# Performance work log

Measured on AMD Instinct MI355X. Metric: run time of the kernel, lower is better.

Reference implementation:

```python
import jax, jax.numpy as jnp
import numpy as np

G, VPG, CPG, LPC = 32, 512, 1024, 3
N_VARS, N_CLAUSES = G * VPG, G * CPG
N_LITS = N_CLAUSES * LPC
FM, QM, ROUNDS = 128, 32, 4
EPS_NORM, EPS_LOG, EPS_SQRT = 1e-6, 1e-8, 1e-6


def _dense_init(key, fin, fout):
    w = jax.random.normal(key, (fin, fout), jnp.float32) * np.float32(np.sqrt(2.0 / (fin + fout)))
    return w, jnp.zeros((fout,), jnp.float32)


def setup_inputs():
    rng = np.random.default_rng(0)
    g_of_clause = np.repeat(np.arange(G), CPG)
    lit_clause = np.repeat(np.arange(N_CLAUSES), LPC).astype(np.int32)
    # each clause picks LPC variables from its own graph's variable block
    lit_var = (np.repeat(g_of_clause * VPG, LPC) + rng.integers(0, VPG, N_LITS)).astype(np.int32)
    lit_sign = (rng.integers(0, 2, N_LITS) * 2 - 1).astype(np.int32)  # +/-1 literal polarity
    variables_mask = np.repeat(np.arange(G), VPG).astype(np.int32)
    clauses_mask = g_of_clause.astype(np.int32)
    keys = jax.random.split(jax.random.key(0), 13)
    inp = dict(
        lit_var=jnp.asarray(lit_var), lit_sign=jnp.asarray(lit_sign), lit_clause=jnp.asarray(lit_clause),
        variables_mask=jnp.asarray(variables_mask), clauses_mask=jnp.asarray(clauses_mask),
        noise=jax.random.normal(keys[12], (ROUNDS, N_VARS, 4), jnp.float32),
    )
    dims = dict(vq=(FM + 4, 2 * QM, QM), cm=(FM + QM, 3 * FM, FM + QM), ug=(FM + 3 * QM, 2 * FM, FM), vo=(FM, FM, 1))
    ki = 0
    for name, (fin, hid, fout) in dims.items():
        for i, (a, b) in enumerate([(fin, hid), (hid, hid), (hid, fout)]):
            w, bb = _dense_init(keys[ki], a, b); ki += 1
            inp[f'{name}_w{i}'] = w
            inp[f'{name}_b{i}'] = bb
    return inp


def _mlp(x, ps):
    # repo MLP: (layer_count-1) hidden Dense with leaky_relu(0.2), linear output, no layer norm
    for w, b in ps[:-1]:
        x = jax.nn.leaky_relu(x @ w + b, negative_slope=0.2)
    w, b = ps[-1]
    return x @ w + b


def _zero_state(n, f):
    # one_hot(0) - 1/f, scaled by sqrt(f)*0.25
    oh = jnp.zeros((n, f), jnp.float32).at[:, 0].set(1.0)
    return (oh - 1.0 / f) * np.float32(np.sqrt(f) * 0.25)


def _forward(lit_var, lit_sign, lit_clause, variables_mask, clauses_mask, noise, params, checkpoint=False):
    p = list(params)
    vq = [(p[0], p[1]), (p[2], p[3]), (p[4], p[5])]
    cm = [(p[6], p[7]), (p[8], p[9]), (p[10], p[11])]
    ug = [(p[12], p[13]), (p[14], p[15]), (p[16], p[17])]
    vo = [(p[18], p[19]), (p[20], p[21]), (p[22], p[23])]
    seg_sum = jax.ops.segment_sum
    sgn = lit_sign.astype(jnp.float32)[:, None]          # [L,1] +/-1
    pos = (sgn > 0).astype(jnp.float32)
    neg = 1.0 - pos
    var_cnt = seg_sum(jnp.ones((N_VARS,), jnp.float32), variables_mask, G)
    cls_cnt = seg_sum(jnp.ones((N_CLAUSES,), jnp.float32), clauses_mask, G)

    def pair_norm(x, seg, cnt):
        mean = seg_sum(x, seg, G) / cnt[:, None]
        x = x - mean[seg]
        return x * jax.lax.rsqrt(jnp.mean(jnp.square(x), axis=-1, keepdims=True) + EPS_NORM)

    def clause_val(q):
        # softplus_loss: V_c = exp(-sum_{lit in c} softplus(sign * q[var]))  -> [N_CLAUSES, d]
        lit = jax.nn.softplus(q[lit_var] * sgn)
        return jnp.exp(-seg_sum(lit, lit_clause, N_CLAUSES))

    def body(carry, noise_t):
        variables, clause_state = carry
        v1 = jnp.concatenate([variables, noise_t], axis=-1)          # [V, FM+4]
        query = _mlp(v1, vq)                                          # [V, QM]

        def q_loss(q):
            cl = clause_val(q)
            return jnp.sum(cl), cl
        variables_grad, clauses_loss = jax.grad(q_loss, has_aux=True)(query)

        clause_data = _mlp(jnp.concatenate([clause_state, clauses_loss], axis=-1), cm)  # [C, FM+QM]
        vloss = clause_data[:, :QM]
        new_cv = pair_norm(clause_data[:, QM:], clauses_mask, cls_cnt) * 0.25
        clause_state = new_cv + 0.1 * clause_state

        contrib = vloss[lit_clause]                                   # [L, QM]
        loss_pos = seg_sum(contrib * pos, lit_var, N_VARS)            # A_pos @ vloss
        loss_neg = seg_sum(contrib * neg, lit_var, N_VARS)            # A_neg @ vloss

        unit = jnp.concatenate([variables, variables_grad, loss_pos, loss_neg], axis=-1)
        new_vars = pair_norm(_mlp(unit, ug), variables_mask, var_cnt) * 0.25
        variables = new_vars + 0.1 * variables

        logits = _mlp(variables, vo)                                  # [V, 1]
        v = clause_val(logits)
        per_clause = v * (-jnp.log(1.0 - v + EPS_LOG))                # softplus_mixed_loss
        per_graph = seg_sum(per_clause, clauses_mask, G)              # [G, 1]
        logit_loss = jnp.sum(jnp.sqrt(per_graph + EPS_SQRT))

        variables = jax.lax.stop_gradient(variables) * 0.2 + variables * 0.8
        clause_state = jax.lax.stop_gradient(clause_state) * 0.2 + clause_state * 0.8
        return (variables, clause_state), (logit_loss, logits)

    if checkpoint:
        body = jax.checkpoint(body)
    init = (_zero_state(N_VARS, FM), _zero_state(N_CLAUSES, FM))
    _, (step_losses, logits_seq) = jax.lax.scan(body, init, noise)
    return logits_seq[-1], jnp.sum(step_losses) / np.float32(ROUNDS)


def reference(lit_var, lit_sign, lit_clause, variables_mask, clauses_mask, noise,
              vq_w0, vq_b0, vq_w1, vq_b1, vq_w2, vq_b2,
              cm_w0, cm_b0, cm_w1, cm_b1, cm_w2, cm_b2,
              ug_w0, ug_b0, ug_w1, ug_b1, ug_w2, ug_b2,
              vo_w0, vo_b0, vo_w1, vo_b1, vo_w2, vo_b2):
    params = (vq_w0, vq_b0, vq_w1, vq_b1, vq_w2, vq_b2,
              cm_w0, cm_b0, cm_w1, cm_b1, cm_w2, cm_b2,
              ug_w0, ug_b0, ug_w1, ug_b1, ug_w2, ug_b2,
              vo_w0, vo_b0, vo_w1, vo_b1, vo_w2, vo_b2)
    return _forward(lit_var, lit_sign, lit_clause, variables_mask, clauses_mask, noise, params)
```

## Files before the change

kernel.cpp:

```cpp
#include <hip/hip_runtime.h>
#include <hip/hip_bf16.h>
#include <math.h>

#define NG     32
#define NVARS  16384
#define NCLS   32768
#define NLITS  98304
#define NROUNDS 4

typedef __attribute__((ext_vector_type(8))) short bf16x8;
typedef __attribute__((ext_vector_type(4))) float f32x4;

#define OFF_VAR    ((size_t)0)
#define OFF_CST    ((size_t)2097152)
#define OFF_XCMB   ((size_t)6291456)
#define OFF_XUGB   ((size_t)9437184)
#define OFF_ABUF   ((size_t)11534336)
#define OFF_BBUF   ((size_t)17825792)
#define OFF_CD     ((size_t)24117248)
#define OFF_Q      ((size_t)30408704)
#define OFF_VG     ((size_t)30932992)
#define OFF_LP     ((size_t)31457280)
#define OFF_LN     ((size_t)31981568)
#define OFF_CMEAN  ((size_t)32505856)
#define OFF_VMEAN  ((size_t)32509952)
#define ZERO_FLOATS ((size_t)1581056)
#define OFF_LOSS   ((size_t)32514048)
#define OFF_WT     ((size_t)32514052)

#define WT_CM0  ((size_t)0)
#define WT_CM1  ((size_t)73728)
#define WT_CM2  ((size_t)221184)
#define WT_UG0  ((size_t)294912)
#define WT_UG1  ((size_t)360448)
#define WT_UG2  ((size_t)425984)
#define WT_VO0  ((size_t)458752)
#define WT_VO1  ((size_t)475136)
#define WT_VQ0  ((size_t)491520)
#define WT_VQ1  ((size_t)501760)
#define WT_VQ2  ((size_t)505856)

__device__ __forceinline__ float softplus_f(float x) {
  return fmaxf(x, 0.f) + log1pf(expf(-fabsf(x)));
}
__device__ __forceinline__ short f2bf(float x) {
  __hip_bfloat16 h = __float2bfloat16(x);
  return *reinterpret_cast<short*>(&h);
}
__device__ __forceinline__ float bf2f(short s) {
  __hip_bfloat16 h = *reinterpret_cast<__hip_bfloat16*>(&s);
  return __bfloat162float(h);
}

__global__ void init_state_kernel(float* __restrict__ var, float* __restrict__ cst,
                                  short* __restrict__ xugb, short* __restrict__ xcmb,
                                  float* __restrict__ loss) {
  int t = blockIdx.x * blockDim.x + threadIdx.x;
  if (t == 0) *loss = 0.f;
  const int main_total = (NVARS + NCLS) * 128;
  if (t < main_total) {
    int row = t >> 7, m = t & 127;
    const float base = 2.82842712474619f;
    float val = ((m == 0) ? (1.f - 1.f / 128.f) : (-1.f / 128.f)) * base;
    if (row < NVARS) {
      var[(size_t)row * 128 + m] = val;
      xugb[(size_t)row * 256 + m] = f2bf(val);
    } else {
      int c = row - NVARS;
      cst[(size_t)c * 128 + m] = val;
      xcmb[(size_t)c * 192 + m] = f2bf(val);
    }
    return;
  }
  int t2 = t - main_total;
  if (t2 < NVARS * 32) {
    int row = t2 >> 5, j = t2 & 31;
    xugb[(size_t)row * 256 + 224 + j] = 0;
    return;
  }
  int t3 = t2 - NVARS * 32;
  if (t3 < NCLS * 32) {
    int row = t3 >> 5, j = t3 & 31;
    xcmb[(size_t)row * 192 + 160 + j] = 0;
  }
}

__global__ void convert_all_kernel(
    const float* __restrict__ cm_w0, const float* __restrict__ cm_w1, const float* __restrict__ cm_w2,
    const float* __restrict__ ug_w0, const float* __restrict__ ug_w1, const float* __restrict__ ug_w2,
    const float* __restrict__ vo_w0, const float* __restrict__ vo_w1,
    const float* __restrict__ vq_w0, const float* __restrict__ vq_w1, const float* __restrict__ vq_w2,
    short* __restrict__ wt) {
  int t = blockIdx.x * blockDim.x + threadIdx.x;
  const float* W; int K, N, Kp; size_t base; int idx;
  if      (t < 73728)  { W = cm_w0; K = 160; N = 384; Kp = 192; base = WT_CM0; idx = t; }
  else if (t < 221184) { W = cm_w1; K = 384; N = 384; Kp = 384; base = WT_CM1; idx = t - 73728; }
  else if (t < 294912) { W = cm_w2; K = 384; N = 160; Kp = 384; base = WT_CM2; idx = t - 221184; }
  else if (t < 360448) { W = ug_w0; K = 224; N = 256; Kp = 256; base = WT_UG0; idx = t - 294912; }
  else if (t < 425984) { W = ug_w1; K = 256; N = 256; Kp = 256; base = WT_UG1; idx = t - 360448; }
  else if (t < 458752) { W = ug_w2; K = 256; N = 128; Kp = 256; base = WT_UG2; idx = t - 425984; }
  else if (t < 475136) { W = vo_w0; K = 128; N = 128; Kp = 128; base = WT_VO0; idx = t - 458752; }
  else if (t < 491520) { W = vo_w1; K = 128; N = 128; Kp = 128; base = WT_VO1; idx = t - 475136; }
  else if (t < 501760) { W = vq_w0; K = 132; N = 64;  Kp = 160; base = WT_VQ0; idx = t - 491520; }
  else if (t < 505856) { W = vq_w1; K = 64;  N = 64;  Kp = 64;  base = WT_VQ1; idx = t - 501760; }
  else if (t < 507904) { W = vq_w2; K = 64;  N = 32;  Kp = 64;  base = WT_VQ2; idx = t - 505856; }
  else return;
  int n = idx / Kp, k = idx - n * Kp;
  float v = (k < K && n < N) ? W[(size_t)k * N + n] : 0.f;
  wt[base + idx] = f2bf(v);
}

__global__ __launch_bounds__(256) void fused_vq_kernel(
    const short* __restrict__ xugb, const float* __restrict__ noise,
    const short* __restrict__ w0, const short* __restrict__ w1, const short* __restrict__ w2,
    const float* __restrict__ b0, const float* __restrict__ b1, const float* __restrict__ b2,
    float* __restrict__ Q, float* __restrict__ zerobase) {
  {
    unsigned gid = blockIdx.x * 256 + threadIdx.x;
    float4 z4 = make_float4(0.f, 0.f, 0.f, 0.f);
    for (size_t i = gid; i < ZERO_FLOATS / 4; i += (size_t)(NVARS / 64) * 256)
      ((float4*)zerobase)[i] = z4;
  }
  __shared__ short A[64 * 160];
  __shared__ short H1[4][16 * 64];
  __shared__ short H2[4][16 * 64];
  const int wid = threadIdx.x >> 6, lane = threadIdx.x & 63;
  const int rbase = blockIdx.x * 64 + wid * 16;
  #pragma unroll
  for (int i = 0; i < 4; ++i) {
    int s = i * 64 + lane;
    int row = s >> 4, c8 = s & 15;
    *(bf16x8*)&A[(wid * 16 + row) * 160 + c8 * 8] =
        *(const bf16x8*)&xugb[(size_t)(rbase + row) * 256 + c8 * 8];
  }
  {
    int row = lane >> 2, seg = lane & 3;
    bf16x8 z = {0, 0, 0, 0, 0, 0, 0, 0};
    if (seg == 0) {
      float4 nz = *(const float4*)&noise[(size_t)(rbase + row) * 4];
      z[0] = f2bf(nz.x); z[1] = f2bf(nz.y); z[2] = f2bf(nz.z); z[3] = f2bf(nz.w);
    }
    *(bf16x8*)&A[(wid * 16 + row) * 160 + 128 + seg * 8] = z;
  }
  const int kof = (lane >> 4) * 8;
  const int l15 = lane & 15;
  f32x4 acc[4] = {};
  #pragma unroll
  for (int ks = 0; ks < 5; ++ks) {
    bf16x8 a = *(const bf16x8*)&A[(wid * 16 + l15) * 160 + ks * 32 + kof];
    #pragma unroll
    for (int ni = 0; ni < 4; ++ni) {
      bf16x8 b = *(const bf16x8*)&w0[(ni * 16 + l15) * 160 + ks * 32 + kof];
      acc[ni] = __builtin_amdgcn_mfma_f32_16x16x32_bf16(a, b, acc[ni], 0, 0, 0);
    }
  }
  #pragma unroll
  for (int ni = 0; ni < 4; ++ni) {
    int col = ni * 16 + l15;
    float bb = b0[col];
    #pragma unroll
    for (int j = 0; j < 4; ++j) {
      float v = acc[ni][j] + bb; v = v > 0.f ? v : 0.2f * v;
      H1[wid][((lane >> 4) * 4 + j) * 64 + col] = f2bf(v);
    }
  }
  f32x4 acc2[4] = {};
  #pragma unroll
  for (int ks = 0; ks < 2; ++ks) {
    bf16x8 a = *(const bf16x8*)&H1[wid][l15 * 64 + ks * 32 + kof];
    #pragma unroll
    for (int ni = 0; ni < 4; ++ni) {
      bf16x8 b = *(const bf16x8*)&w1[(ni * 16 + l15) * 64 + ks * 32 + kof];
      acc2[ni] = __builtin_amdgcn_mfma_f32_16x16x32_bf16(a, b, acc2[ni], 0, 0, 0);
    }
  }
  #pragma unroll
  for (int ni = 0; ni < 4; ++ni) {
    int col = ni * 16 + l15;
    float bb = b1[col];
    #pragma unroll
    for (int j = 0; j < 4; ++j) {
      float v = acc2[ni][j] + bb; v = v > 0.f ? v : 0.2f * v;
      H2[wid][((lane >> 4) * 4 + j) * 64 + col] = f2bf(v);
    }
  }
  f32x4 acc3[2] = {};
  #pragma unroll
  for (int ks = 0; ks < 2; ++ks) {
    bf16x8 a = *(const bf16x8*)&H2[wid][l15 * 64 + ks * 32 + kof];
    #pragma unroll
    for (int ni = 0; ni < 2; ++ni) {
      bf16x8 b = *(const bf16x8*)&w2[(ni * 16 + l15) * 64 + ks * 32 + kof];
      acc3[ni] = __builtin_amdgcn_mfma_f32_16x16x32_bf16(a, b, acc3[ni], 0, 0, 0);
    }
  }
  #pragma unroll
  for (int ni = 0; ni < 2; ++ni) {
    int col = ni * 16 + l15;
    float bb = b2[col];
    #pragma unroll
    for (int j = 0; j < 4; ++j)
      Q[(size_t)(rbase + (lane >> 4) * 4 + j) * 32 + col] = acc3[ni][j] + bb;
  }
}

__global__ void fused_clause_kernel(const float* __restrict__ Q, const int* __restrict__ lit_var,
                                    const int* __restrict__ lit_sign,
                                    short* __restrict__ xcmb, float* __restrict__ vg) {
  int t = blockIdx.x * blockDim.x + threadIdx.x;
  if (t >= NCLS * 32) return;
  int c = t >> 5, m = t & 31;
  int l0 = 3 * c;
  int v0 = lit_var[l0], v1 = lit_var[l0 + 1], v2 = lit_var[l0 + 2];
  int s0 = lit_sign[l0], s1 = lit_sign[l0 + 1], s2 = lit_sign[l0 + 2];
  float q0 = Q[(size_t)v0 * 32 + m];
  float q1 = Q[(size_t)v1 * 32 + m];
  float q2 = Q[(size_t)v2 * 32 + m];
  float sp = softplus_f(q0 * (float)s0) + softplus_f(q1 * (float)s1) + softplus_f(q2 * (float)s2);
  float cl = expf(-sp);
  xcmb[(size_t)c * 192 + 128 + m] = f2bf(cl);
  float g0 = 1.f / (1.f + expf(-q0)) - (s0 < 0 ? 1.f : 0.f);
  float g1 = 1.f / (1.f + expf(-q1)) - (s1 < 0 ? 1.f : 0.f);
  float g2 = 1.f / (1.f + expf(-q2)) - (s2 < 0 ? 1.f : 0.f);
  atomicAdd(&vg[(size_t)v0 * 32 + m], -cl * g0);
  atomicAdd(&vg[(size_t)v1 * 32 + m], -cl * g1);
  atomicAdd(&vg[(size_t)v2 * 32 + m], -cl * g2);
}

template<int TN, bool RELU, bool OUTBF16, int EPI>
__global__ __launch_bounds__(256) void gemm_mfma_kernel(
    const short* __restrict__ A, int lda,
    const short* __restrict__ Wt,
    const float* __restrict__ bias, int nbias,
    void* __restrict__ Cout, int Np, int Kp,
    const int* __restrict__ lit_var, const int* __restrict__ lit_sign,
    float* __restrict__ lp, float* __restrict__ ln,
    float* __restrict__ meanbuf, float inv_cnt, int gshift) {
  constexpr int NB = TN / 32;
  __shared__ short As[128 * 64];
  __shared__ short Bs[TN * 64];
  const int bn = blockIdx.x * TN;
  const int bm = blockIdx.y * 128;
  const int tid  = threadIdx.x;
  const int wid  = tid >> 6;
  const int lane = tid & 63;
  const int wm = (wid >> 1) * 64;
  const int wn = (wid & 1) * (TN / 2);

  f32x4 acc[4][NB] = {};

  for (int k0 = 0; k0 < Kp; k0 += 64) {
    #pragma unroll
    for (int i = 0; i < 4; ++i) {
      int s = (i * 4 + wid) * 64 + lane;
      int row = s >> 3, cs = (s & 7) << 3;
      const short* src = A + (size_t)(bm + row) * lda + k0 + cs;
      __builtin_amdgcn_global_load_lds(
          (const __attribute__((address_space(1))) void*)src,
          (__attribute__((address_space(3))) void*)(As + (size_t)(i * 4 + wid) * 64 * 8),
          16, 0, 0);
    }
    #pragma unroll
    for (int i = 0; i < TN / 32; ++i) {
      int s = (i * 4 + wid) * 64 + lane;
      int n = s >> 3, cs = (s & 7) << 3;
      const short* src = Wt + (size_t)(bn + n) * Kp + k0 + cs;
      __builtin_amdgcn_global_load_lds(
          (const __attribute__((address_space(1))) void*)src,
          (__attribute__((address_space(3))) void*)(Bs + (size_t)(i * 4 + wid) * 64 * 8),
          16, 0, 0);
    }
    __syncthreads();

    #pragma unroll
    for (int ks = 0; ks < 2; ++ks) {
      const int kof = ks * 32 + (lane >> 4) * 8;
      bf16x8 a[4], b[NB];
      #pragma unroll
      for (int mi = 0; mi < 4; ++mi)
        a[mi] = *(const bf16x8*)&As[(wm + mi * 16 + (lane & 15)) * 64 + kof];
      #pragma unroll
      for (int ni = 0; ni < NB; ++ni)
        b[ni] = *(const bf16x8*)&Bs[(wn + ni * 16 + (lane & 15)) * 64 + kof];
      #pragma unroll
      for (int mi = 0; mi < 4; ++mi)
        #pragma unroll
        for (int ni = 0; ni < NB; ++ni)
          acc[mi][ni] = __builtin_amdgcn_mfma_f32_16x16x32_bf16(a[mi], b[ni], acc[mi][ni], 0, 0, 0);
    }
    __syncthreads();
  }

  const int col0 = bn + wn + (lane & 15);
  const int row0 = bm + wm + (lane >> 4) * 4;
  #pragma unroll
  for (int ni = 0; ni < NB; ++ni) {
    int col = col0 + ni * 16;
    float bv = (col < nbias) ? bias[col] : 0.f;
    float colsum = 0.f;
    #pragma unroll
    for (int mi = 0; mi < 4; ++mi) {
      #pragma unroll
      for (int j = 0; j < 4; ++j) {
        int row = row0 + mi * 16 + j;
        float v = acc[mi][ni][j] + bv;
        if (EPI == 0) {
          if (RELU) v = v > 0.f ? v : 0.2f * v;
          if (OUTBF16) ((short*)Cout)[(size_t)row * Np + col] = f2bf(v);
          else         ((float*)Cout)[(size_t)row * Np + col] = v;
        } else if (EPI == 1) {
          if (col < 32) {
            #pragma unroll
            for (int i = 0; i < 3; ++i) {
              int l = 3 * row + i;
              int vv = lit_var[l];
              float* tgt = (lit_sign[l] > 0) ? lp : ln;
              atomicAdd(&tgt[(size_t)vv * 32 + col], v);
            }
          } else if (col < 160) {
            ((float*)Cout)[(size_t)row * Np + col] = v;
            colsum += v;
          }
        } else {
          ((float*)Cout)[(size_t)row * Np + col] = v;
          colsum += v;
        }
      }
    }
    if ((EPI == 1 && col >= 32 && col < 160) || EPI == 2) {
      colsum += __shfl_xor(colsum, 16);
      colsum += __shfl_xor(colsum, 32);
      if ((lane >> 4) == 0) {
        int midx = (EPI == 1) ? (col - 32) : col;
        atomicAdd(&meanbuf[(size_t)(bm >> gshift) * 128 + midx], colsum * inv_cnt);
      }
    }
  }
}

__global__ __launch_bounds__(256) void pairnorm_update_kernel(
    const float* __restrict__ x, int stride, int coloff,
    const float* __restrict__ mean, float* __restrict__ state,
    short* __restrict__ bout, int bstride, int rows_per_g) {
  int wid = threadIdx.x >> 6;
  int lane = threadIdx.x & 63;
  int row = blockIdx.x * 4 + wid;
  int g = row / rows_per_g;
  const float* xp = x + (size_t)row * stride + coloff;
  float y0 = xp[lane]      - mean[g * 128 + lane];
  float y1 = xp[lane + 64] - mean[g * 128 + lane + 64];
  float ss = y0 * y0 + y1 * y1;
  #pragma unroll
  for (int o = 32; o > 0; o >>= 1) ss += __shfl_xor(ss, o);
  float inv = rsqrtf(ss * (1.f / 128.f) + 1e-6f);
  float* sp = state + (size_t)row * 128;
  float s0 = y0 * inv * 0.25f + 0.1f * sp[lane];
  float s1 = y1 * inv * 0.25f + 0.1f * sp[lane + 64];
  sp[lane]      = s0;
  sp[lane + 64] = s1;
  bout[(size_t)row * bstride + lane]      = f2bf(s0);
  bout[(size_t)row * bstride + lane + 64] = f2bf(s1);
}

__global__ void xug_tail_kernel(const float* __restrict__ vg, const float* __restrict__ lp,
                                const float* __restrict__ ln, short* __restrict__ xugb) {
  int t = blockIdx.x * blockDim.x + threadIdx.x;
  if (t >= NVARS * 128) return;
  int v = t >> 7, j = t & 127;
  if (j >= 96) return;
  float x;
  if (j < 32)       x = vg[(size_t)v * 32 + j];
  else if (j < 64)  x = lp[(size_t)v * 32 + (j - 32)];
  else              x = ln[(size_t)v * 32 + (j - 64)];
  xugb[(size_t)v * 256 + 128 + j] = f2bf(x);
}

__global__ __launch_bounds__(256) void fused_vo_kernel(
    const short* __restrict__ xugb,
    const short* __restrict__ w0, const short* __restrict__ w1,
    const float* __restrict__ b0, const float* __restrict__ b1,
    const float* __restrict__ w2, const float* __restrict__ b2,
    float* __restrict__ logits) {
  __shared__ short A[64 * 128];
  __shared__ short H1[4][16 * 128];
  __shared__ short H2[4][16 * 128];
  const int wid = threadIdx.x >> 6, lane = threadIdx.x & 63;
  const int rbase = blockIdx.x * 64 + wid * 16;
  #pragma unroll
  for (int i = 0; i < 4; ++i) {
    int s = i * 64 + lane;
    int row = s >> 4, c8 = s & 15;
    *(bf16x8*)&A[(wid * 16 + row) * 128 + c8 * 8] =
        *(const bf16x8*)&xugb[(size_t)(rbase + row) * 256 + c8 * 8];
  }
  const int kof = (lane >> 4) * 8;
  const int l15 = lane & 15;
  f32x4 acc[8] = {};
  #pragma unroll
  for (int ks = 0; ks < 4; ++ks) {
    bf16x8 a = *(const bf16x8*)&A[(wid * 16 + l15) * 128 + ks * 32 + kof];
    #pragma unroll
    for (int ni = 0; ni < 8; ++ni) {
      bf16x8 b = *(const bf16x8*)&w0[(ni * 16 + l15) * 128 + ks * 32 + kof];
      acc[ni] = __builtin_amdgcn_mfma_f32_16x16x32_bf16(a, b, acc[ni], 0, 0, 0);
    }
  }
  #pragma unroll
  for (int ni = 0; ni < 8; ++ni) {
    int col = ni * 16 + l15;
    float bb = b0[col];
    #pragma unroll
    for (int j = 0; j < 4; ++j) {
      float v = acc[ni][j] + bb; v = v > 0.f ? v : 0.2f * v;
      H1[wid][((lane >> 4) * 4 + j) * 128 + col] = f2bf(v);
    }
  }
  f32x4 acc2[8] = {};
  #pragma unroll
  for (int ks = 0; ks < 4; ++ks) {
    bf16x8 a = *(const bf16x8*)&H1[wid][l15 * 128 + ks * 32 + kof];
    #pragma unroll
    for (int ni = 0; ni < 8; ++ni) {
      bf16x8 b = *(const bf16x8*)&w1[(ni * 16 + l15) * 128 + ks * 32 + kof];
      acc2[ni] = __builtin_amdgcn_mfma_f32_16x16x32_bf16(a, b, acc2[ni], 0, 0, 0);
    }
  }
  #pragma unroll
  for (int ni = 0; ni < 8; ++ni) {
    int col = ni * 16 + l15;
    float bb = b1[col];
    #pragma unroll
    for (int j = 0; j < 4; ++j) {
      float v = acc2[ni][j] + bb; v = v > 0.f ? v : 0.2f * v;
      H2[wid][((lane >> 4) * 4 + j) * 128 + col] = f2bf(v);
    }
  }
  {
    int row = lane >> 2, q = lane & 3;
    float s = 0.f;
    #pragma unroll
    for (int jj = 0; jj < 4; ++jj) {
      bf16x8 h = *(const bf16x8*)&H2[wid][row * 128 + q * 32 + jj * 8];
      #pragma unroll
      for (int e = 0; e < 8; ++e) s += bf2f(h[e]) * w2[q * 32 + jj * 8 + e];
    }
    s += __shfl_xor(s, 1);
    s += __shfl_xor(s, 2);
    if (q == 0) logits[rbase + row] = s + b2[0];
  }
}

__global__ __launch_bounds__(1024) void fused_loss_kernel(
    const float* __restrict__ logits, const int* __restrict__ lit_var,
    const int* __restrict__ lit_sign, float* __restrict__ loss) {
  __shared__ float lg[512];
  __shared__ float red[16];
  int g = blockIdx.x, tid = threadIdx.x;
  if (tid < 512) lg[tid] = logits[(size_t)g * 512 + tid];
  __syncthreads();
  int c = g * 1024 + tid;
  float s = 0.f;
  #pragma unroll
  for (int i = 0; i < 3; ++i) {
    int l = 3 * c + i;
    float sg = (float)lit_sign[l];
    s += softplus_f(lg[lit_var[l] - g * 512] * sg);
  }
  float vv = expf(-s);
  float pcv = vv * (-logf(1.f - vv + 1e-8f));
  #pragma unroll
  for (int o = 32; o > 0; o >>= 1) pcv += __shfl_xor(pcv, o);
  if ((tid & 63) == 0) red[tid >> 6] = pcv;
  __syncthreads();
  if (tid < 16) {
    float x = red[tid];
    #pragma unroll
    for (int o = 8; o > 0; o >>= 1) x += __shfl_xor(x, o);
    if (tid == 0) atomicAdd(loss, sqrtf(x + 1e-6f));
  }
}

__global__ void finalize_kernel(const float* __restrict__ loss_acc, float* __restrict__ out) {
  out[0] = loss_acc[0] * 0.25f;
}

extern "C" void kernel_launch(void* const* d_in, const int* in_sizes, int n_in,
                              void* d_out, int out_size, void* d_ws, size_t ws_size,
                              hipStream_t stream) {
  const int* lit_var    = (const int*)d_in[0];
  const int* lit_sign   = (const int*)d_in[1];
  const float* noise    = (const float*)d_in[5];
  const float* vq_w0 = (const float*)d_in[6];   const float* vq_b0 = (const float*)d_in[7];
  const float* vq_w1 = (const float*)d_in[8];   const float* vq_b1 = (const float*)d_in[9];
  const float* vq_w2 = (const float*)d_in[10];  const float* vq_b2 = (const float*)d_in[11];
  const float* cm_w0 = (const float*)d_in[12];  const float* cm_b0 = (const float*)d_in[13];
  const float* cm_w1 = (const float*)d_in[14];  const float* cm_b1 = (const float*)d_in[15];
  const float* cm_w2 = (const float*)d_in[16];  const float* cm_b2 = (const float*)d_in[17];
  const float* ug_w0 = (const float*)d_in[18];  const float* ug_b0 = (const float*)d_in[19];
  const float* ug_w1 = (const float*)d_in[20];  const float* ug_b1 = (const float*)d_in[21];
  const float* ug_w2 = (const float*)d_in[22];  const float* ug_b2 = (const float*)d_in[23];
  const float* vo_w0 = (const float*)d_in[24];  const float* vo_b0 = (const float*)d_in[25];
  const float* vo_w1 = (const float*)d_in[26];  const float* vo_b1 = (const float*)d_in[27];
  const float* vo_w2 = (const float*)d_in[28];  const float* vo_b2 = (const float*)d_in[29];

  float* ws = (float*)d_ws;
  float* var   = ws + OFF_VAR;
  float* cst   = ws + OFF_CST;
  short* xcmb  = (short*)(ws + OFF_XCMB);
  short* xugb  = (short*)(ws + OFF_XUGB);
  short* bufA  = (short*)(ws + OFF_ABUF);
  short* bufB  = (short*)(ws + OFF_BBUF);
  float* CD    = ws + OFF_CD;
  float* Q     = ws + OFF_Q;
  float* vg    = ws + OFF_VG;
  float* lp    = ws + OFF_LP;
  float* ln    = ws + OFF_LN;
  float* cmean = ws + OFF_CMEAN;
  float* vmean = ws + OFF_VMEAN;
  float* loss  = ws + OFF_LOSS;
  short* wt    = (short*)(ws + OFF_WT);
  float* logits = (float*)d_out;
  float* loss_out = (float*)d_out + NVARS;

  convert_all_kernel<<<1984, 256, 0, stream>>>(cm_w0, cm_w1, cm_w2, ug_w0, ug_w1, ug_w2,
                                               vo_w0, vo_w1, vq_w0, vq_w1, vq_w2, wt);
  init_state_kernel<<<30720, 256, 0, stream>>>(var, cst, xugb, xcmb, loss);

  for (int r = 0; r < NROUNDS; ++r) {
    const float* noise_r = noise + (size_t)r * NVARS * 4;

    fused_vq_kernel<<<NVARS / 64, 256, 0, stream>>>(
        xugb, noise_r, wt + WT_VQ0, wt + WT_VQ1, wt + WT_VQ2, vq_b0, vq_b1, vq_b2, Q, vg);

    fused_clause_kernel<<<NCLS * 32 / 256, 256, 0, stream>>>(Q, lit_var, lit_sign, xcmb, vg);

    gemm_mfma_kernel<128, true, true, 0><<<dim3(3, NCLS / 128), 256, 0, stream>>>(
        xcmb, 192, wt + WT_CM0, cm_b0, 384, bufA, 384, 192,
        nullptr, nullptr, nullptr, nullptr, nullptr, 0.f, 0);
    gemm_mfma_kernel<128, true, true, 0><<<dim3(3, NCLS / 128), 256, 0, stream>>>(
        bufA, 384, wt + WT_CM1, cm_b1, 384, bufB, 384, 384,
        nullptr, nullptr, nullptr, nullptr, nullptr, 0.f, 0);
    gemm_mfma_kernel<64, false, false, 1><<<dim3(3, NCLS / 128), 256, 0, stream>>>(
        bufB, 384, wt + WT_CM2, cm_b2, 160, CD, 192, 384,
        lit_var, lit_sign, lp, ln, cmean, 1.f / 1024.f, 10);

    pairnorm_update_kernel<<<NCLS / 4, 256, 0, stream>>>(CD, 192, 32, cmean, cst, xcmb, 192, 1024);

    xug_tail_kernel<<<NVARS * 128 / 256, 256, 0, stream>>>(vg, lp, ln, xugb);

    gemm_mfma_kernel<128, true, true, 0><<<dim3(2, NVARS / 128), 256, 0, stream>>>(
        xugb, 256, wt + WT_UG0, ug_b0, 256, bufA, 256, 256,
        nullptr, nullptr, nullptr, nullptr, nullptr, 0.f, 0);
    gemm_mfma_kernel<128, true, true, 0><<<dim3(2, NVARS / 128), 256, 0, stream>>>(
        bufA, 256, wt + WT_UG1, ug_b1, 256, bufB, 256, 256,
        nullptr, nullptr, nullptr, nullptr, nullptr, 0.f, 0);
    gemm_mfma_kernel<64, false, false, 2><<<dim3(2, NVARS / 128), 256, 0, stream>>>(
        bufB, 256, wt + WT_UG2, ug_b2, 128, CD, 128, 256,
        nullptr, nullptr, nullptr, nullptr, vmean, 1.f / 512.f, 9);

    pairnorm_update_kernel<<<NVARS / 4, 256, 0, stream>>>(CD, 128, 0, vmean, var, xugb, 256, 512);

    fused_vo_kernel<<<NVARS / 64, 256, 0, stream>>>(
        xugb, wt + WT_VO0, wt + WT_VO1, vo_b0, vo_b1, vo_w2, vo_b2, logits);

    fused_loss_kernel<<<NG, 1024, 0, stream>>>(logits, lit_var, lit_sign, loss);
  }

  finalize_kernel<<<1, 1, 0, stream>>>(loss, loss_out);
}
```

Measured before the change: 719.1 us.

## Replace clause-to-variable scatter atomics with CSR gather and fuse pairnorm with tail

Builds a variable-to-literal CSR index once per call (count, scan, fill kernels). Each round then gathers clause values per variable instead of atomically scattering vg, lp and ln from the clause kernel and the GEMM epilogue. The per-round zeroing of those buffers disappears; only the mean buffers are cleared, inside the clause kernel. The clause pairnorm and the xug tail build become one launch. This removes float atomics and a zero pass, at the cost of three setup launches, one of them a single-block scan, and an irregular, variable-length gather loop per variable.

New measurement: 682.1 us. 5.1% less time.

```diff
diff --git a/kernel.cpp b/kernel.cpp
--- a/kernel.cpp
+++ b/kernel.cpp
@@ -19,14 +19,15 @@
 #define OFF_BBUF   ((size_t)17825792)
 #define OFF_CD     ((size_t)24117248)
 #define OFF_Q      ((size_t)30408704)
-#define OFF_VG     ((size_t)30932992)
-#define OFF_LP     ((size_t)31457280)
-#define OFF_LN     ((size_t)31981568)
-#define OFF_CMEAN  ((size_t)32505856)
-#define OFF_VMEAN  ((size_t)32509952)
-#define ZERO_FLOATS ((size_t)1581056)
-#define OFF_LOSS   ((size_t)32514048)
-#define OFF_WT     ((size_t)32514052)
+#define OFF_CLF    ((size_t)30932992)
+#define OFF_VLOSS  ((size_t)31981568)
+#define OFF_CMEAN  ((size_t)33030144)
+#define OFF_VMEAN  ((size_t)33034240)
+#define OFF_LOSS   ((size_t)33038336)
+#define OFF_CSO    ((size_t)33038340)
+#define OFF_CSE    ((size_t)33054725)
+#define OFF_CSC    ((size_t)33153029)
+#define OFF_WT     ((size_t)33169416)
 
 #define WT_CM0  ((size_t)0)
 #define WT_CM1  ((size_t)73728)
@@ -54,7 +55,7 @@
 
 __global__ void init_state_kernel(float* __restrict__ var, float* __restrict__ cst,
                                   short* __restrict__ xugb, short* __restrict__ xcmb,
-                                  float* __restrict__ loss) {
+                                  float* __restrict__ loss, int* __restrict__ cnt) {
   int t = blockIdx.x * blockDim.x + threadIdx.x;
   if (t == 0) *loss = 0.f;
   const int main_total = (NVARS + NCLS) * 128;
@@ -82,7 +83,54 @@
   if (t3 < NCLS * 32) {
     int row = t3 >> 5, j = t3 & 31;
     xcmb[(size_t)row * 192 + 160 + j] = 0;
-  }
+    return;
+  }
+  int t4 = t3 - NCLS * 32;
+  if (t4 < NVARS) cnt[t4] = 0;
+}
+
+__global__ void csr_count_kernel(const int* __restrict__ lit_var, int* __restrict__ cnt) {
+  int l = blockIdx.x * blockDim.x + threadIdx.x;
+  if (l >= NLITS) return;
+  atomicAdd(&cnt[lit_var[l]], 1);
+}
+
+__global__ __launch_bounds__(1024) void csr_scan_kernel(const int* __restrict__ cnt,
+                                                        int* __restrict__ cso,
+                                                        int* __restrict__ cur) {
+  __shared__ int part[1024];
+  int t = threadIdx.x;
+  int base = t * 16;
+  int local[16];
+  int s = 0;
+  #pragma unroll
+  for (int i = 0; i < 16; ++i) { local[i] = cnt[base + i]; s += local[i]; }
+  part[t] = s;
+  __syncthreads();
+  for (int off = 1; off < 1024; off <<= 1) {
+    int v = (t >= off) ? part[t - off] : 0;
+    __syncthreads();
+    part[t] += v;
+    __syncthreads();
+  }
+  int run = part[t] - s;
+  #pragma unroll
+  for (int i = 0; i < 16; ++i) {
+    cso[base + i] = run;
+    cur[base + i] = run;
+    run += local[i];
+  }
+  if (t == 1023) cso[NVARS] = run;
+}
+
+__global__ void csr_fill_kernel(const int* __restrict__ lit_var, const int* __restrict__ lit_sign,
+                                const int* __restrict__ lit_clause,
+                                int* __restrict__ cur, int* __restrict__ cse) {
+  int l = blockIdx.x * blockDim.x + threadIdx.x;
+  if (l >= NLITS) return;
+  int v = lit_var[l];
+  int pos = atomicAdd(&cur[v], 1);
+  cse[pos] = (lit_clause[l] << 1) | (lit_sign[l] > 0 ? 1 : 0);
 }
 
 __global__ void convert_all_kernel(
@@ -114,13 +162,7 @@
     const short* __restrict__ xugb, const float* __restrict__ noise,
     const short* __restrict__ w0, const short* __restrict__ w1, const short* __restrict__ w2,
     const float* __restrict__ b0, const float* __restrict__ b1, const float* __restrict__ b2,
-    float* __restrict__ Q, float* __restrict__ zerobase) {
-  {
-    unsigned gid = blockIdx.x * 256 + threadIdx.x;
-    float4 z4 = make_float4(0.f, 0.f, 0.f, 0.f);
-    for (size_t i = gid; i < ZERO_FLOATS / 4; i += (size_t)(NVARS / 64) * 256)
-      ((float4*)zerobase)[i] = z4;
-  }
+    float* __restrict__ Q) {
   __shared__ short A[64 * 160];
   __shared__ short H1[4][16 * 64];
   __shared__ short H2[4][16 * 64];
@@ -206,8 +248,10 @@
 
 __global__ void fused_clause_kernel(const float* __restrict__ Q, const int* __restrict__ lit_var,
                                     const int* __restrict__ lit_sign,
-                                    short* __restrict__ xcmb, float* __restrict__ vg) {
+                                    short* __restrict__ xcmb, float* __restrict__ clf,
+                                    float* __restrict__ meanz) {
   int t = blockIdx.x * blockDim.x + threadIdx.x;
+  if (t < 2 * 32 * 128) meanz[t] = 0.f;
   if (t >= NCLS * 32) return;
   int c = t >> 5, m = t & 31;
   int l0 = 3 * c;
@@ -218,13 +262,8 @@
   float q2 = Q[(size_t)v2 * 32 + m];
   float sp = softplus_f(q0 * (float)s0) + softplus_f(q1 * (float)s1) + softplus_f(q2 * (float)s2);
   float cl = expf(-sp);
+  clf[(size_t)c * 32 + m] = cl;
   xcmb[(size_t)c * 192 + 128 + m] = f2bf(cl);
-  float g0 = 1.f / (1.f + expf(-q0)) - (s0 < 0 ? 1.f : 0.f);
-  float g1 = 1.f / (1.f + expf(-q1)) - (s1 < 0 ? 1.f : 0.f);
-  float g2 = 1.f / (1.f + expf(-q2)) - (s2 < 0 ? 1.f : 0.f);
-  atomicAdd(&vg[(size_t)v0 * 32 + m], -cl * g0);
-  atomicAdd(&vg[(size_t)v1 * 32 + m], -cl * g1);
-  atomicAdd(&vg[(size_t)v2 * 32 + m], -cl * g2);
 }
 
 template<int TN, bool RELU, bool OUTBF16, int EPI>
@@ -233,8 +272,7 @@
     const short* __restrict__ Wt,
     const float* __restrict__ bias, int nbias,
     void* __restrict__ Cout, int Np, int Kp,
-    const int* __restrict__ lit_var, const int* __restrict__ lit_sign,
-    float* __restrict__ lp, float* __restrict__ ln,
+    float* __restrict__ aux,
     float* __restrict__ meanbuf, float inv_cnt, int gshift) {
   constexpr int NB = TN / 32;
   __shared__ short As[128 * 64];
@@ -310,13 +348,7 @@
           else         ((float*)Cout)[(size_t)row * Np + col] = v;
         } else if (EPI == 1) {
           if (col < 32) {
-            #pragma unroll
-            for (int i = 0; i < 3; ++i) {
-              int l = 3 * row + i;
-              int vv = lit_var[l];
-              float* tgt = (lit_sign[l] > 0) ? lp : ln;
-              atomicAdd(&tgt[(size_t)vv * 32 + col], v);
-            }
+            aux[(size_t)row * 32 + col] = v;
           } else if (col < 160) {
             ((float*)Cout)[(size_t)row * Np + col] = v;
             colsum += v;
@@ -335,6 +367,55 @@
         atomicAdd(&meanbuf[(size_t)(bm >> gshift) * 128 + midx], colsum * inv_cnt);
       }
     }
+  }
+}
+
+__global__ __launch_bounds__(256) void pnc_gather_kernel(
+    const float* __restrict__ CD, const float* __restrict__ cmean,
+    float* __restrict__ cst, short* __restrict__ xcmb,
+    const float* __restrict__ Q, const int* __restrict__ cso, const int* __restrict__ cse,
+    const float* __restrict__ clf, const float* __restrict__ vloss,
+    short* __restrict__ xugb) {
+  int b = blockIdx.x;
+  if (b < NCLS / 4) {
+    int wid = threadIdx.x >> 6;
+    int lane = threadIdx.x & 63;
+    int row = b * 4 + wid;
+    int g = row >> 10;
+    const float* xp = CD + (size_t)row * 192 + 32;
+    float y0 = xp[lane]      - cmean[g * 128 + lane];
+    float y1 = xp[lane + 64] - cmean[g * 128 + lane + 64];
+    float ss = y0 * y0 + y1 * y1;
+    #pragma unroll
+    for (int o = 32; o > 0; o >>= 1) ss += __shfl_xor(ss, o);
+    float inv = rsqrtf(ss * (1.f / 128.f) + 1e-6f);
+    float* sp = cst + (size_t)row * 128;
+    float s0 = y0 * inv * 0.25f + 0.1f * sp[lane];
+    float s1 = y1 * inv * 0.25f + 0.1f * sp[lane + 64];
+    sp[lane]      = s0;
+    sp[lane + 64] = s1;
+    xcmb[(size_t)row * 192 + lane]      = f2bf(s0);
+    xcmb[(size_t)row * 192 + lane + 64] = f2bf(s1);
+  } else {
+    int t = (b - NCLS / 4) * 256 + threadIdx.x;
+    int v = t >> 5, m = t & 31;
+    float q = Q[(size_t)v * 32 + m];
+    float sig = 1.f / (1.f + expf(-q));
+    float vgs = 0.f, lps = 0.f, lns = 0.f;
+    int e0 = cso[v], e1 = cso[v + 1];
+    for (int e = e0; e < e1; ++e) {
+      int ent = cse[e];
+      int c = ent >> 1;
+      bool pos = ent & 1;
+      float clc = clf[(size_t)c * 32 + m];
+      vgs -= clc * (sig - (pos ? 0.f : 1.f));
+      float vl = vloss[(size_t)c * 32 + m];
+      if (pos) lps += vl; else lns += vl;
+    }
+    short* xp = xugb + (size_t)v * 256 + 128;
+    xp[m]      = f2bf(vgs);
+    xp[32 + m] = f2bf(lps);
+    xp[64 + m] = f2bf(lns);
   }
 }
 
@@ -362,19 +443,6 @@
   bout[(size_t)row * bstride + lane + 64] = f2bf(s1);
 }
 
-__global__ void xug_tail_kernel(const float* __restrict__ vg, const float* __restrict__ lp,
-                                const float* __restrict__ ln, short* __restrict__ xugb) {
-  int t = blockIdx.x * blockDim.x + threadIdx.x;
-  if (t >= NVARS * 128) return;
-  int v = t >> 7, j = t & 127;
-  if (j >= 96) return;
-  float x;
-  if (j < 32)       x = vg[(size_t)v * 32 + j];
-  else if (j < 64)  x = lp[(size_t)v * 32 + (j - 32)];
-  else              x = ln[(size_t)v * 32 + (j - 64)];
-  xugb[(size_t)v * 256 + 128 + j] = f2bf(x);
-}
-
 __global__ __launch_bounds__(256) void fused_vo_kernel(
     const short* __restrict__ xugb,
     const short* __restrict__ w0, const short* __restrict__ w1,
@@ -489,6 +557,7 @@
                               hipStream_t stream) {
   const int* lit_var    = (const int*)d_in[0];
   const int* lit_sign   = (const int*)d_in[1];
+  const int* lit_clause = (const int*)d_in[2];
   const float* noise    = (const float*)d_in[5];
   const float* vq_w0 = (const float*)d_in[6];   const float* vq_b0 = (const float*)d_in[7];
   const float* vq_w1 = (const float*)d_in[8];   const float* vq_b1 = (const float*)d_in[9];
@@ -512,51 +581,49 @@
   short* bufB  = (short*)(ws + OFF_BBUF);
   float* CD    = ws + OFF_CD;
   float* Q     = ws + OFF_Q;
-  float* vg    = ws + OFF_VG;
-  float* lp    = ws + OFF_LP;
-  float* ln    = ws + OFF_LN;
+  float* clf   = ws + OFF_CLF;
+  float* vloss = ws + OFF_VLOSS;
   float* cmean = ws + OFF_CMEAN;
   float* vmean = ws + OFF_VMEAN;
   float* loss  = ws + OFF_LOSS;
+  int*   cso   = (int*)(ws + OFF_CSO);
+  int*   cse   = (int*)(ws + OFF_CSE);
+  int*   csc   = (int*)(ws + OFF_CSC);
   short* wt    = (short*)(ws + OFF_WT);
   float* logits = (float*)d_out;
   float* loss_out = (float*)d_out + NVARS;
 
   convert_all_kernel<<<1984, 256, 0, stream>>>(cm_w0, cm_w1, cm_w2, ug_w0, ug_w1, ug_w2,
                                                vo_w0, vo_w1, vq_w0, vq_w1, vq_w2, wt);
-  init_state_kernel<<<30720, 256, 0, stream>>>(var, cst, xugb, xcmb, loss);
+  init_state_kernel<<<30784, 256, 0, stream>>>(var, cst, xugb, xcmb, loss, csc);
+  csr_count_kernel<<<NLITS / 256, 256, 0, stream>>>(lit_var, csc);
+  csr_scan_kernel<<<1, 1024, 0, stream>>>(csc, cso, csc);
+  csr_fill_kernel<<<NLITS / 256, 256, 0, stream>>>(lit_var, lit_sign, lit_clause, csc, cse);
 
   for (int r = 0; r < NROUNDS; ++r) {
     const float* noise_r = noise + (size_t)r * NVARS * 4;
 
     fused_vq_kernel<<<NVARS / 64, 256, 0, stream>>>(
-        xugb, noise_r, wt + WT_VQ0, wt + WT_VQ1, wt + WT_VQ2, vq_b0, vq_b1, vq_b2, Q, vg);
-
-    fused_clause_kernel<<<NCLS * 32 / 256, 256, 0, stream>>>(Q, lit_var, lit_sign, xcmb, vg);
+        xugb, noise_r, wt + WT_VQ0, wt + WT_VQ1, wt + WT_VQ2, vq_b0, vq_b1, vq_b2, Q);
+
+    fused_clause_kernel<<<NCLS * 32 / 256, 256, 0, stream>>>(Q, lit_var, lit_sign, xcmb, clf, cmean);
 
     gemm_mfma_kernel<128, true, true, 0><<<dim3(3, NCLS / 128), 256, 0, stream>>>(
-        xcmb, 192, wt + WT_CM0, cm_b0, 384, bufA, 384, 192,
-        nullptr, nullptr, nullptr, nullptr, nullptr, 0.f, 0);
+        xcmb, 192, wt + WT_CM0, cm_b0, 384, bufA, 384, 192, nullptr, nullptr, 0.f, 0);
     gemm_mfma_kernel<128, true, true, 0><<<dim3(3, NCLS / 128), 256, 0, stream>>>(
-        bufA, 384, wt + WT_CM1, cm_b1, 384, bufB, 384, 384,
-        nullptr, nullptr, nullptr, nullptr, nullptr, 0.f, 0);
+        bufA, 384, wt + WT_CM1, cm_b1, 384, bufB, 384, 384, nullptr, nullptr, 0.f, 0);
     gemm_mfma_kernel<64, false, false, 1><<<dim3(3, NCLS / 128), 256, 0, stream>>>(
-        bufB, 384, wt + WT_CM2, cm_b2, 160, CD, 192, 384,
-        lit_var, lit_sign, lp, ln, cmean, 1.f / 1024.f, 10);
-
-    pairnorm_update_kernel<<<NCLS / 4, 256, 0, stream>>>(CD, 192, 32, cmean, cst, xcmb, 192, 1024);
-
-    xug_tail_kernel<<<NVARS * 128 / 256, 256, 0, stream>>>(vg, lp, ln, xugb);
+        bufB, 384, wt + WT_CM2, cm_b2, 160, CD, 192, 384, vloss, cmean, 1.f / 1024.f, 10);
+
+    pnc_gather_kernel<<<NCLS / 4 + NVARS * 32 / 256, 256, 0, stream>>>(
+        CD, cmean, cst, xcmb, Q, cso, cse, clf, vloss, xugb);
 
     gemm_mfma_kernel<128, true, true, 0><<<dim3(2, NVARS / 128), 256, 0, stream>>>(
-        xugb, 256, wt + WT_UG0, ug_b0, 256, bufA, 256, 256,
-        nullptr, nullptr, nullptr, nullptr, nullptr, 0.f, 0);
+        xugb, 256, wt + WT_UG0, ug_b0, 256, bufA, 256, 256, nullptr, nullptr, 0.f, 0);
     gemm_mfma_kernel<128, true, true, 0><<<dim3(2, NVARS / 128), 256, 0, stream>>>(
-        bufA, 256, wt + WT_UG1, ug_b1, 256, bufB, 256, 256,
-        nullptr, nullptr, nullptr, nullptr, nullptr, 0.f, 0);
+        bufA, 256, wt + WT_UG1, ug_b1, 256, bufB, 256, 256, nullptr, nullptr, 0.f, 0);
     gemm_mfma_kernel<64, false, false, 2><<<dim3(2, NVARS / 128), 256, 0, stream>>>(
-        bufB, 256, wt + WT_UG2, ug_b2, 128, CD, 128, 256,
-        nullptr, nullptr, nullptr, nullptr, vmean, 1.f / 512.f, 9);
+        bufB, 256, wt + WT_UG2, ug_b2, 128, CD, 128, 256, nullptr, vmean, 1.f / 512.f, 9);
 
     pairnorm_update_kernel<<<NVARS / 4, 256, 0, stream>>>(CD, 128, 0, vmean, var, xugb, 256, 512);
 
```
